# Optimization experiments

Measured on AMD Instinct MI355X. Metric: run time of the kernel, lower is better.

## Reference

```python
import jax, jax.numpy as jnp
import numpy as np

B, N, S, F = 16384, 1152, 576, 8  # batch, n_sites, n_symm, features
LOG2 = float(np.log(2.0))


def log_cosh(x):
    # numerically stable log(cosh(x)) = |x| + log1p(exp(-2|x|)) - log(2)
    a = jnp.abs(x)
    return a + jnp.log1p(jnp.exp(-2.0 * a)) - LOG2


def setup_inputs() -> dict:
    key = jax.random.key(0)
    ks = iter(jax.random.split(key, 32))
    f32 = jnp.float32
    d = {}
    d['x'] = jax.random.normal(next(ks), (B, N), dtype=f32)
    d['symmetries'] = jax.random.randint(next(ks), (S, N), 0, N, dtype=jnp.int32)
    d['corr0'] = jax.random.randint(next(ks), (576, 4), 0, N, dtype=jnp.int32)
    d['corr1'] = jax.random.randint(next(ks), (576, 4), 0, N, dtype=jnp.int32)
    d['corr2'] = jax.random.randint(next(ks), (24, 24), 0, N, dtype=jnp.int32)
    d['corr3'] = jax.random.randint(next(ks), (24, 24), 0, N, dtype=jnp.int32)
    d['corr0_symm'] = jax.random.randint(next(ks), (S, 576), 0, 576, dtype=jnp.int32)
    d['corr1_symm'] = jax.random.randint(next(ks), (S, 576), 0, 576, dtype=jnp.int32)
    d['corr2_symm'] = jax.random.randint(next(ks), (S, 24), 0, 24, dtype=jnp.int32)
    d['corr3_symm'] = jax.random.randint(next(ks), (S, 24), 0, 24, dtype=jnp.int32)
    std = 0.01
    d['hidden_bias'] = std * jax.random.normal(next(ks), (F,), dtype=f32)
    d['symm_kernel'] = std * jax.random.normal(next(ks), (F, N), dtype=f32)
    d['visible_bias'] = std * jax.random.normal(next(ks), (2,), dtype=f32)
    d['corr0_bias'] = std * jax.random.normal(next(ks), (1,), dtype=f32)
    d['corr0_kernel'] = std * jax.random.normal(next(ks), (F, 576), dtype=f32)
    d['corr1_bias'] = std * jax.random.normal(next(ks), (1,), dtype=f32)
    d['corr1_kernel'] = std * jax.random.normal(next(ks), (F, 576), dtype=f32)
    d['corr2_bias'] = std * jax.random.normal(next(ks), (1,), dtype=f32)
    d['corr2_kernel'] = std * jax.random.normal(next(ks), (F, 24), dtype=f32)
    d['corr3_bias'] = std * jax.random.normal(next(ks), (1,), dtype=f32)
    d['corr3_kernel'] = std * jax.random.normal(next(ks), (F, 24), dtype=f32)
    d['loop0_hidden_bias'] = std * jax.random.normal(next(ks), (F,), dtype=f32)
    d['loop0_kernel'] = std * jax.random.normal(next(ks), (F, 24), dtype=f32)
    d['loop1_hidden_bias'] = std * jax.random.normal(next(ks), (F,), dtype=f32)
    d['loop1_kernel'] = std * jax.random.normal(next(ks), (F, 24), dtype=f32)
    return d


def reference(x, symmetries, corr0, corr1, corr2, corr3,
              corr0_symm, corr1_symm, corr2_symm, corr3_symm,
              hidden_bias, symm_kernel, visible_bias,
              corr0_bias, corr0_kernel, corr1_bias, corr1_kernel,
              corr2_bias, corr2_kernel, corr3_bias, corr3_kernel,
              loop0_hidden_bias, loop0_kernel, loop1_hidden_bias, loop1_kernel):
    n_batch = x.shape[0]
    # symmetrized kernel: (F, S, N)
    K = jnp.take(symm_kernel, symmetries, axis=1)
    theta = jnp.einsum('bn,fsn->bfs', x, K)  # (B, F, S)
    theta = theta + hidden_bias[:, None]
    bias = jnp.sum(x.reshape(n_batch, -1, 2), axis=1) @ visible_bias  # (B,)

    correlators = [corr0, corr1, corr2, corr3]
    corr_symms = [corr0_symm, corr1_symm, corr2_symm, corr3_symm]
    corr_biases = [corr0_bias, corr1_bias, corr2_bias, corr3_bias]
    corr_kernels = [corr0_kernel, corr1_kernel, corr2_kernel, corr3_kernel]

    corr_values = []
    for corr, csym, cb, ck in zip(correlators, corr_symms, corr_biases, corr_kernels):
        ckk = jnp.take(ck, csym, axis=1)               # (F, S, C)
        cv = jnp.take(x, corr, axis=1).prod(axis=2)    # (B, C)
        corr_values.append(cv)
        theta = theta + jnp.einsum('bc,fsc->bfs', cv, ckk)
        bias = bias + cb * jnp.sum(cv, axis=1)

    out = jnp.sum(log_cosh(theta), axis=(1, 2))  # (B,)

    # last two correlators are loop correlators with dedicated hidden units
    loop_params = [(loop0_hidden_bias, loop0_kernel, corr2_symm, corr_values[2]),
                   (loop1_hidden_bias, loop1_kernel, corr3_symm, corr_values[3])]
    for lhb, lk, lsym, lv in loop_params:
        lkk = jnp.take(lk, lsym, axis=1)                      # (F, S, C)
        lt = jnp.einsum('bc,fsc->bfs', lv, lkk) + lhb[:, None]
        out = out + jnp.sum(log_cosh(lt), axis=(1, 2))

    return out + bias
```

## Files before the change

kernel.cpp:

```cpp
#include <hip/hip_runtime.h>
#include <math.h>

#define B_    16384
#define N_    1152
#define KPAD  2496
#define NKT32 78
#define KLOOP 256
#define NOUT  4608
#define NT2   18
#define LOG2F_ 0.69314718055994530942f

typedef unsigned short ushort_t;
typedef __attribute__((ext_vector_type(8))) short short8;
typedef __attribute__((ext_vector_type(4))) float floatx4;

__device__ __forceinline__ float log_cosh_f(float t) {
    float a = fabsf(t);
    return a + __logf(1.0f + __expf(-2.0f * a)) - LOG2F_;
}
__device__ __forceinline__ ushort_t bf16_rne(float f) {
    unsigned int u = __float_as_uint(f);
    return (ushort_t)((u + 0x7fffu + ((u >> 16) & 1u)) >> 16);
}
__device__ __forceinline__ float bf16_to_f(ushort_t h) {
    return __uint_as_float(((unsigned int)h) << 16);
}

typedef __attribute__((address_space(1))) const unsigned int guint;
typedef __attribute__((address_space(3))) unsigned int luint;
__device__ __forceinline__ void gload16(const ushort_t* src, ushort_t* dst) {
    __builtin_amdgcn_global_load_lds((guint*)src, (luint*)dst, 16, 0, 0);
}

__global__ __launch_bounds__(256) void build_w(
    const int* __restrict__ symm,
    const int* __restrict__ c0s, const int* __restrict__ c1s,
    const int* __restrict__ c2s, const int* __restrict__ c3s,
    const float* __restrict__ sk,
    const float* __restrict__ ck0, const float* __restrict__ ck1,
    const float* __restrict__ ck2, const float* __restrict__ ck3,
    const float* __restrict__ l0k, const float* __restrict__ l1k,
    ushort_t* __restrict__ Wb, ushort_t* __restrict__ LWb)
{
    __shared__ int idx[2352];
    const int s = blockIdx.x;
    const int tid = threadIdx.x;
    for (int i = tid; i < 1152; i += 256) idx[i] = symm[s * N_ + i];
    for (int i = tid; i < 576; i += 256) idx[1152 + i] = c0s[s * 576 + i];
    for (int i = tid; i < 576; i += 256) idx[1728 + i] = c1s[s * 576 + i];
    if (tid < 24) idx[2304 + tid] = c2s[s * 24 + tid];
    else if (tid < 48) idx[2328 + (tid - 24)] = c3s[s * 24 + (tid - 24)];
    __syncthreads();
    for (int f = 0; f < 8; ++f) {
        ushort_t* wr = Wb + (size_t)(s * 8 + f) * KPAD;
        for (int k = tid; k < KPAD; k += 256) {
            ushort_t o;
            if (k < 1152)      o = bf16_rne(sk[f * N_ + idx[k]]);
            else if (k < 1728) o = bf16_rne(ck0[f * 576 + idx[k]]);
            else if (k < 2304) o = bf16_rne(ck1[f * 576 + idx[k]]);
            else if (k < 2448) {
                int q = k - 2304, g = q / 48, c = q - g * 48;
                float w = (c < 24) ? ck2[f * 24 + idx[2304 + c]]
                                   : ck3[f * 24 + idx[2328 + (c - 24)]];
                ushort_t hi = bf16_rne(w);
                o = (g < 2) ? hi : bf16_rne(w - bf16_to_f(hi));
            } else o = 0;
            wr[k] = o;
        }
        ushort_t* lr = LWb + (size_t)(s * 8 + f) * KLOOP;
        for (int k2 = tid; k2 < KLOOP; k2 += 256) {
            int j2 = k2 >> 7, q = k2 & 127;
            ushort_t o = 0;
            if (q < 72) {
                int g = q / 24, c = q - g * 24;
                float w = j2 ? l1k[f * 24 + idx[2328 + c]]
                             : l0k[f * 24 + idx[2304 + c]];
                ushort_t hi = bf16_rne(w);
                o = (g < 2) ? hi : bf16_rne(w - bf16_to_f(hi));
            }
            lr[k2] = o;
        }
    }
}

__global__ __launch_bounds__(256) void build_cv(
    const float* __restrict__ x,
    const int* __restrict__ corr0, const int* __restrict__ corr1,
    const int* __restrict__ corr2, const int* __restrict__ corr3,
    const float* __restrict__ vb,
    const float* __restrict__ cb0, const float* __restrict__ cb1,
    const float* __restrict__ cb2, const float* __restrict__ cb3,
    ushort_t* __restrict__ XA, ushort_t* __restrict__ CVL,
    float* __restrict__ initb)
{
    __shared__ float xs[N_];
    __shared__ float red[256];
    __shared__ float cvhi[48], cvlo[48];
    const int tid = threadIdx.x;
    const int b = blockIdx.x;
    ushort_t* xr = XA + (size_t)b * KPAD;

    float bias = 0.f;
    const float vb0 = vb[0], vb1 = vb[1];
    for (int i = tid; i < N_; i += 256) {
        float v = x[(size_t)b * N_ + i];
        xs[i] = v;
        bias += v * ((i & 1) ? vb1 : vb0);
        xr[i] = bf16_rne(v);
    }
    __syncthreads();
    float s0 = 0.f, s1 = 0.f, s2 = 0.f, s3 = 0.f;
    for (int c = tid; c < 576; c += 256) {
        const int* i0 = corr0 + c * 4;
        float p = xs[i0[0]] * xs[i0[1]] * xs[i0[2]] * xs[i0[3]];
        xr[1152 + c] = bf16_rne(p); s0 += p;
        const int* i1 = corr1 + c * 4;
        float q = xs[i1[0]] * xs[i1[1]] * xs[i1[2]] * xs[i1[3]];
        xr[1728 + c] = bf16_rne(q); s1 += q;
    }
    if (tid < 48) {
        int j2 = tid / 24, c = tid - j2 * 24;
        const int* ii = (j2 ? corr3 : corr2) + c * 24;
        float p = 1.f;
        for (int j = 0; j < 24; ++j) p *= xs[ii[j]];
        float hv = bf16_to_f(bf16_rne(p));
        cvhi[tid] = hv;
        cvlo[tid] = p - hv;
        if (j2) s3 = p; else s2 = p;
    }
    __syncthreads();
    for (int i = tid; i < KPAD - 2304; i += 256) {
        ushort_t o = 0;
        if (i < 144) {
            int g = i / 48, c = i - g * 48;
            o = bf16_rne(g == 1 ? cvlo[c] : cvhi[c]);
        }
        xr[2304 + i] = o;
    }
    ushort_t* cr = CVL + (size_t)b * KLOOP;
    for (int k2 = tid; k2 < KLOOP; k2 += 256) {
        int j2 = k2 >> 7, q = k2 & 127;
        ushort_t o = 0;
        if (q < 72) {
            int g = q / 24, c = q - g * 24;
            o = bf16_rne(g == 1 ? cvlo[j2 * 24 + c] : cvhi[j2 * 24 + c]);
        }
        cr[k2] = o;
    }
    bias += cb0[0] * s0 + cb1[0] * s1 + cb2[0] * s2 + cb3[0] * s3;
    red[tid] = bias;
    __syncthreads();
    for (int off = 128; off; off >>= 1) {
        if (tid < off) red[tid] += red[tid + off];
        __syncthreads();
    }
    if (tid == 0) initb[b] = red[0];
}

__global__ __launch_bounds__(512, 4) void mfma_gemm(
    const ushort_t* __restrict__ XA, const ushort_t* __restrict__ Wb,
    const ushort_t* __restrict__ CVL, const ushort_t* __restrict__ LWb,
    const float* __restrict__ hidden_bias,
    const float* __restrict__ l0hb, const float* __restrict__ l1hb,
    float* __restrict__ partials)
{
    __shared__ __align__(16) ushort_t sh[36864];
    __shared__ float redsh[640];

    const int tid = threadIdx.x;
    const int l = tid & 63, w = tid >> 6;
    const int wm = w >> 2, wn = w & 3;
    const int lrow = l & 15, lg = l >> 4;
    const int srow = l >> 2;
    const int sgr8 = ((l & 3) ^ ((srow >> 1) & 3)) * 8;

    const int bid = blockIdx.x;
    const int swz = (bid & 7) * 288 + (bid >> 3);
    const int nt = swz >> 7, bt = swz & 127;
    const int n0 = nt * 256, b0 = bt * 128;

    const ushort_t* XAb  = XA  + (size_t)b0 * KPAD;
    const ushort_t* Wbb  = Wb  + (size_t)n0 * KPAD;
    const ushort_t* CVb  = CVL + (size_t)b0 * KLOOP;
    const ushort_t* LWbb = LWb + (size_t)n0 * KLOOP;

    floatx4 acc[4][4];

    auto STGA = [&](const ushort_t* g, int stride, int kg, int bo) {
        gload16(g + (size_t)(w * 16 + srow) * stride + kg + sgr8,
                &sh[bo + w * 16 * 32]);
    };
    auto STGB = [&](const ushort_t* g, int stride, int kg, int bo) {
#pragma unroll
        for (int i = 0; i < 2; ++i) {
            const int r0 = i * 128 + w * 16;
            gload16(g + (size_t)(r0 + srow) * stride + kg + sgr8,
                    &sh[bo + 4096 + r0 * 32]);
        }
    };

    const int ga = (lg ^ ((lrow >> 1) & 3)) * 8;
    const int abase = (wm * 64 + lrow) * 32 + ga;
    const int bbase = 4096 + (wn * 64 + lrow) * 32 + ga;

    auto TILE = [&](int bo) {
        short8 af[4], bfr[4];
#pragma unroll
        for (int mi = 0; mi < 4; ++mi)
            af[mi] = *(const short8*)&sh[bo + abase + mi * 512];
#pragma unroll
        for (int ni = 0; ni < 4; ++ni)
            bfr[ni] = *(const short8*)&sh[bo + bbase + ni * 512];
        __builtin_amdgcn_s_setprio(1);
#pragma unroll
        for (int mi = 0; mi < 4; ++mi)
#pragma unroll
            for (int ni = 0; ni < 4; ++ni)
                acc[mi][ni] = __builtin_amdgcn_mfma_f32_16x16x32_bf16(
                    af[mi], bfr[ni], acc[mi][ni], 0, 0, 0);
        __builtin_amdgcn_s_setprio(0);
    };

#pragma unroll
    for (int mi = 0; mi < 4; ++mi)
#pragma unroll
        for (int ni = 0; ni < 4; ++ni) acc[mi][ni] = (floatx4){0.f, 0.f, 0.f, 0.f};

    int c0 = 0, c1 = 12288, c2 = 24576;
    STGA(XAb, KPAD, 0, c0);  STGB(Wbb, KPAD, 0, c0);
    STGA(XAb, KPAD, 32, c1); STGB(Wbb, KPAD, 32, c1);
#pragma unroll 1
    for (int t = 0; t < NKT32 - 1; ++t) {
        asm volatile("s_waitcnt vmcnt(3)" ::: "memory");
        __builtin_amdgcn_s_barrier();
        if (t < NKT32 - 2) {
            STGA(XAb, KPAD, (t + 2) * 32, c2);
            STGB(Wbb, KPAD, (t + 2) * 32, c2);
        }
        TILE(c0);
        int tmp = c0; c0 = c1; c1 = c2; c2 = tmp;
    }
    asm volatile("s_waitcnt vmcnt(0)" ::: "memory");
    __builtin_amdgcn_s_barrier();
    TILE(c0);

    {
        const float hbv = hidden_bias[l & 7];
#pragma unroll
        for (int mi = 0; mi < 4; ++mi)
#pragma unroll
            for (int reg = 0; reg < 4; ++reg) {
                float v = 0.f;
#pragma unroll
                for (int ni = 0; ni < 4; ++ni)
                    v += log_cosh_f(acc[mi][ni][reg] + hbv);
                v += __shfl_xor(v, 1);
                v += __shfl_xor(v, 2);
                v += __shfl_xor(v, 4);
                v += __shfl_xor(v, 8);
                if (lrow == 0)
                    redsh[(wm * 64 + mi * 16 + lg * 4 + reg) * 5 + wn] = v;
            }
    }

#pragma unroll 1
    for (int j2 = 0; j2 < 2; ++j2) {
#pragma unroll
        for (int mi = 0; mi < 4; ++mi)
#pragma unroll
            for (int ni = 0; ni < 4; ++ni) acc[mi][ni] = (floatx4){0.f, 0.f, 0.f, 0.f};
        __syncthreads();
        const int kb = j2 * 128;
        STGA(CVb, KLOOP, kb, 0);          STGB(LWbb, KLOOP, kb, 0);
        STGA(CVb, KLOOP, kb + 32, 12288); STGB(LWbb, KLOOP, kb + 32, 12288);
        int m0 = 0, m1 = 12288, m2 = 24576;
#pragma unroll 1
        for (int t = 0; t < 4; ++t) {
            if (t < 3) asm volatile("s_waitcnt vmcnt(3)" ::: "memory");
            else       asm volatile("s_waitcnt vmcnt(0)" ::: "memory");
            __builtin_amdgcn_s_barrier();
            if (t < 2) {
                STGA(CVb, KLOOP, kb + (t + 2) * 32, m2);
                STGB(LWbb, KLOOP, kb + (t + 2) * 32, m2);
            }
            TILE(m0);
            int tmp = m0; m0 = m1; m1 = m2; m2 = tmp;
        }
        const float lbv = (j2 ? l1hb : l0hb)[l & 7];
#pragma unroll
        for (int mi = 0; mi < 4; ++mi)
#pragma unroll
            for (int reg = 0; reg < 4; ++reg) {
                float v = 0.f;
#pragma unroll
                for (int ni = 0; ni < 4; ++ni)
                    v += log_cosh_f(acc[mi][ni][reg] + lbv);
                v += __shfl_xor(v, 1);
                v += __shfl_xor(v, 2);
                v += __shfl_xor(v, 4);
                v += __shfl_xor(v, 8);
                if (lrow == 0)
                    redsh[(wm * 64 + mi * 16 + lg * 4 + reg) * 5 + wn] += v;
            }
    }

    __syncthreads();
    if (tid < 128) {
        float t = redsh[tid * 5 + 0] + redsh[tid * 5 + 1] +
                  redsh[tid * 5 + 2] + redsh[tid * 5 + 3];
        partials[(size_t)nt * B_ + b0 + tid] = t;
    }
}

__global__ __launch_bounds__(256) void finalize_out(
    const float* __restrict__ initb, const float* __restrict__ partials,
    float* __restrict__ out)
{
    int b = blockIdx.x * 256 + threadIdx.x;
    float s = initb[b];
#pragma unroll
    for (int t = 0; t < NT2; ++t) s += partials[(size_t)t * B_ + b];
    out[b] = s;
}

extern "C" void kernel_launch(void* const* d_in, const int* in_sizes, int n_in,
                              void* d_out, int out_size, void* d_ws, size_t ws_size,
                              hipStream_t stream) {
    const float* x    = (const float*)d_in[0];
    const int* symm   = (const int*)d_in[1];
    const int* corr0  = (const int*)d_in[2];
    const int* corr1  = (const int*)d_in[3];
    const int* corr2  = (const int*)d_in[4];
    const int* corr3  = (const int*)d_in[5];
    const int* c0s    = (const int*)d_in[6];
    const int* c1s    = (const int*)d_in[7];
    const int* c2s    = (const int*)d_in[8];
    const int* c3s    = (const int*)d_in[9];
    const float* hb   = (const float*)d_in[10];
    const float* sk   = (const float*)d_in[11];
    const float* vb   = (const float*)d_in[12];
    const float* cb0  = (const float*)d_in[13];
    const float* ck0  = (const float*)d_in[14];
    const float* cb1  = (const float*)d_in[15];
    const float* ck1  = (const float*)d_in[16];
    const float* cb2  = (const float*)d_in[17];
    const float* ck2  = (const float*)d_in[18];
    const float* cb3  = (const float*)d_in[19];
    const float* ck3  = (const float*)d_in[20];
    const float* l0hb = (const float*)d_in[21];
    const float* l0k  = (const float*)d_in[22];
    const float* l1hb = (const float*)d_in[23];
    const float* l1k  = (const float*)d_in[24];

    ushort_t* wsu = (ushort_t*)d_ws;
    ushort_t* Wb  = wsu;
    ushort_t* XA  = Wb + (size_t)NOUT * KPAD;
    ushort_t* LWb = XA + (size_t)B_ * KPAD;
    ushort_t* CVL = LWb + (size_t)NOUT * KLOOP;
    float* initb    = (float*)(CVL + (size_t)B_ * KLOOP);
    float* partials = initb + B_;

    build_w<<<576, 256, 0, stream>>>(
        symm, c0s, c1s, c2s, c3s, sk, ck0, ck1, ck2, ck3, l0k, l1k, Wb, LWb);
    build_cv<<<B_, 256, 0, stream>>>(
        x, corr0, corr1, corr2, corr3, vb, cb0, cb1, cb2, cb3, XA, CVL, initb);
    mfma_gemm<<<2304, 512, 0, stream>>>(
        XA, Wb, CVL, LWb, hb, l0hb, l1hb, partials);
    finalize_out<<<B_ / 256, 256, 0, stream>>>(initb, partials, (float*)d_out);
}
```

Baseline: 579.5 us.

## Enlarge GEMM tile to 256x256 with 32x32 MFMA and four-stage LDS pipeline

The main bf16 GEMM now computes a 256x256 output tile per block instead of 128x256, using 32x32x16 MFMA instructions with a 4x2 accumulator grid per wave. The K loop becomes a four-buffer LDS pipeline with register double-buffering of fragments, so LDS reads overlap MFMA issue. The padded K is raised to a multiple of 128 so the loop splits evenly into phases. The goal is more data reuse per loaded byte and higher MFMA throughput. In exchange it uses far more LDS, which cuts occupancy, launches half as many blocks, which may leave a tail of partly idle CUs, and adds a little padded-K work.

```diff
diff --git a/kernel.cpp b/kernel.cpp
--- a/kernel.cpp
+++ b/kernel.cpp
@@ -3,8 +3,8 @@
 
 #define B_    16384
 #define N_    1152
-#define KPAD  2496
-#define NKT32 78
+#define KPAD  2560
+#define NKT   80
 #define KLOOP 256
 #define NOUT  4608
 #define NT2   18
@@ -12,7 +12,7 @@
 
 typedef unsigned short ushort_t;
 typedef __attribute__((ext_vector_type(8))) short short8;
-typedef __attribute__((ext_vector_type(4))) float floatx4;
+typedef __attribute__((ext_vector_type(16))) float floatx16;
 
 __device__ __forceinline__ float log_cosh_f(float t) {
     float a = fabsf(t);
@@ -157,155 +157,171 @@
     if (tid == 0) initb[b] = red[0];
 }
 
-__global__ __launch_bounds__(512, 4) void mfma_gemm(
+__global__ __launch_bounds__(512, 2) void mfma_gemm(
     const ushort_t* __restrict__ XA, const ushort_t* __restrict__ Wb,
     const ushort_t* __restrict__ CVL, const ushort_t* __restrict__ LWb,
     const float* __restrict__ hidden_bias,
     const float* __restrict__ l0hb, const float* __restrict__ l1hb,
     float* __restrict__ partials)
 {
-    __shared__ __align__(16) ushort_t sh[36864];
-    __shared__ float redsh[640];
+    __shared__ __align__(16) ushort_t sh[65536];
+    __shared__ float redsh[1280];
 
     const int tid = threadIdx.x;
     const int l = tid & 63, w = tid >> 6;
     const int wm = w >> 2, wn = w & 3;
-    const int lrow = l & 15, lg = l >> 4;
+    const int l31 = l & 31, lh = l >> 5;
     const int srow = l >> 2;
     const int sgr8 = ((l & 3) ^ ((srow >> 1) & 3)) * 8;
 
     const int bid = blockIdx.x;
-    const int swz = (bid & 7) * 288 + (bid >> 3);
-    const int nt = swz >> 7, bt = swz & 127;
-    const int n0 = nt * 256, b0 = bt * 128;
+    const int swz = (bid & 7) * 144 + (bid >> 3);
+    const int nt = swz % NT2, bt = swz / NT2;
+    const int n0 = nt * 256, b0 = bt * 256;
 
     const ushort_t* XAb  = XA  + (size_t)b0 * KPAD;
     const ushort_t* Wbb  = Wb  + (size_t)n0 * KPAD;
     const ushort_t* CVb  = CVL + (size_t)b0 * KLOOP;
     const ushort_t* LWbb = LWb + (size_t)n0 * KLOOP;
 
-    floatx4 acc[4][4];
-
-    auto STGA = [&](const ushort_t* g, int stride, int kg, int bo) {
-        gload16(g + (size_t)(w * 16 + srow) * stride + kg + sgr8,
-                &sh[bo + w * 16 * 32]);
-    };
-    auto STGB = [&](const ushort_t* g, int stride, int kg, int bo) {
+    const int fsw = (l31 >> 1) & 3;
+    const int ao0 = l31 * 32 + (((0 + lh) ^ fsw) * 8);
+    const int ao1 = l31 * 32 + (((2 + lh) ^ fsw) * 8);
+    const int aBase = wm * 4096;
+    const int bBase = 8192 + wn * 2048;
+
+    floatx16 acc[4][2];
+    short8 aX[4], bX[2], aY[4], bY[2];
+
+    auto STGA = [&](const ushort_t* g, int stride, int kg, int bufbase) {
 #pragma unroll
         for (int i = 0; i < 2; ++i) {
             const int r0 = i * 128 + w * 16;
             gload16(g + (size_t)(r0 + srow) * stride + kg + sgr8,
-                    &sh[bo + 4096 + r0 * 32]);
-        }
-    };
-
-    const int ga = (lg ^ ((lrow >> 1) & 3)) * 8;
-    const int abase = (wm * 64 + lrow) * 32 + ga;
-    const int bbase = 4096 + (wn * 64 + lrow) * 32 + ga;
-
-    auto TILE = [&](int bo) {
-        short8 af[4], bfr[4];
-#pragma unroll
-        for (int mi = 0; mi < 4; ++mi)
-            af[mi] = *(const short8*)&sh[bo + abase + mi * 512];
-#pragma unroll
-        for (int ni = 0; ni < 4; ++ni)
-            bfr[ni] = *(const short8*)&sh[bo + bbase + ni * 512];
+                    &sh[bufbase + r0 * 32]);
+        }
+    };
+    auto STAGE = [&](int kg, int bufbase) {
+        STGA(XAb, KPAD, kg, bufbase);
+        STGA(Wbb, KPAD, kg, bufbase + 8192);
+    };
+    auto RD = [&](int bufbase, int ao, short8* a, short8* b) {
+#pragma unroll
+        for (int mi = 0; mi < 4; ++mi)
+            a[mi] = *(const short8*)&sh[bufbase + aBase + mi * 1024 + ao];
+#pragma unroll
+        for (int ni = 0; ni < 2; ++ni)
+            b[ni] = *(const short8*)&sh[bufbase + bBase + ni * 1024 + ao];
+    };
+    auto MM = [&](short8* a, short8* b) {
         __builtin_amdgcn_s_setprio(1);
 #pragma unroll
         for (int mi = 0; mi < 4; ++mi)
 #pragma unroll
-            for (int ni = 0; ni < 4; ++ni)
-                acc[mi][ni] = __builtin_amdgcn_mfma_f32_16x16x32_bf16(
-                    af[mi], bfr[ni], acc[mi][ni], 0, 0, 0);
+            for (int ni = 0; ni < 2; ++ni)
+                acc[mi][ni] = __builtin_amdgcn_mfma_f32_32x32x16_bf16(
+                    a[mi], b[ni], acc[mi][ni], 0, 0, 0);
         __builtin_amdgcn_s_setprio(0);
     };
-
-#pragma unroll
-    for (int mi = 0; mi < 4; ++mi)
-#pragma unroll
-        for (int ni = 0; ni < 4; ++ni) acc[mi][ni] = (floatx4){0.f, 0.f, 0.f, 0.f};
-
-    int c0 = 0, c1 = 12288, c2 = 24576;
-    STGA(XAb, KPAD, 0, c0);  STGB(Wbb, KPAD, 0, c0);
-    STGA(XAb, KPAD, 32, c1); STGB(Wbb, KPAD, 32, c1);
+    auto ZACC = [&]() {
+#pragma unroll
+        for (int mi = 0; mi < 4; ++mi)
+#pragma unroll
+            for (int ni = 0; ni < 2; ++ni)
+#pragma unroll
+                for (int r = 0; r < 16; ++r) acc[mi][ni][r] = 0.f;
+    };
+
+    ZACC();
+
+    STAGE(0, 0); STAGE(32, 16384); STAGE(64, 32768);
+    asm volatile("s_waitcnt vmcnt(8)" ::: "memory");
+    __builtin_amdgcn_sched_barrier(0);
+    __builtin_amdgcn_s_barrier();
+    RD(0, ao0, aX, bX);
+
 #pragma unroll 1
-    for (int t = 0; t < NKT32 - 1; ++t) {
-        asm volatile("s_waitcnt vmcnt(3)" ::: "memory");
-        __builtin_amdgcn_s_barrier();
-        if (t < NKT32 - 2) {
-            STGA(XAb, KPAD, (t + 2) * 32, c2);
-            STGB(Wbb, KPAD, (t + 2) * 32, c2);
-        }
-        TILE(c0);
-        int tmp = c0; c0 = c1; c1 = c2; c2 = tmp;
-    }
-    asm volatile("s_waitcnt vmcnt(0)" ::: "memory");
-    __builtin_amdgcn_s_barrier();
-    TILE(c0);
+    for (int tb = 0; tb < 19; ++tb) {
+#pragma unroll
+        for (int ph = 0; ph < 4; ++ph) {
+            const int t = tb * 4 + ph;
+            const int cb = ph * 16384;
+            const int nb = ((ph + 3) & 3) * 16384;
+            const int b1 = ((ph + 1) & 3) * 16384;
+            RD(cb, ao1, aY, bY);
+            STAGE((t + 3) * 32, nb);
+            MM(aX, bX);
+            asm volatile("s_waitcnt vmcnt(8) lgkmcnt(0)" ::: "memory");
+            __builtin_amdgcn_sched_barrier(0);
+            __builtin_amdgcn_s_barrier();
+            RD(b1, ao0, aX, bX);
+            MM(aY, bY);
+        }
+    }
+    RD(0, ao1, aY, bY); STAGE(79 * 32, 49152); MM(aX, bX);
+    asm volatile("s_waitcnt vmcnt(8) lgkmcnt(0)" ::: "memory");
+    __builtin_amdgcn_sched_barrier(0); __builtin_amdgcn_s_barrier();
+    RD(16384, ao0, aX, bX); MM(aY, bY);
+    RD(16384, ao1, aY, bY); MM(aX, bX);
+    asm volatile("s_waitcnt vmcnt(4) lgkmcnt(0)" ::: "memory");
+    __builtin_amdgcn_sched_barrier(0); __builtin_amdgcn_s_barrier();
+    RD(32768, ao0, aX, bX); MM(aY, bY);
+    RD(32768, ao1, aY, bY); MM(aX, bX);
+    asm volatile("s_waitcnt vmcnt(0) lgkmcnt(0)" ::: "memory");
+    __builtin_amdgcn_sched_barrier(0); __builtin_amdgcn_s_barrier();
+    RD(49152, ao0, aX, bX); MM(aY, bY);
+    RD(49152, ao1, aY, bY); MM(aX, bX); MM(aY, bY);
 
     {
         const float hbv = hidden_bias[l & 7];
 #pragma unroll
         for (int mi = 0; mi < 4; ++mi)
 #pragma unroll
-            for (int reg = 0; reg < 4; ++reg) {
-                float v = 0.f;
-#pragma unroll
-                for (int ni = 0; ni < 4; ++ni)
-                    v += log_cosh_f(acc[mi][ni][reg] + hbv);
-                v += __shfl_xor(v, 1);
-                v += __shfl_xor(v, 2);
-                v += __shfl_xor(v, 4);
-                v += __shfl_xor(v, 8);
-                if (lrow == 0)
-                    redsh[(wm * 64 + mi * 16 + lg * 4 + reg) * 5 + wn] = v;
+            for (int reg = 0; reg < 16; ++reg) {
+                float v = log_cosh_f(acc[mi][0][reg] + hbv)
+                        + log_cosh_f(acc[mi][1][reg] + hbv);
+                v += __shfl_xor(v, 1);  v += __shfl_xor(v, 2);
+                v += __shfl_xor(v, 4);  v += __shfl_xor(v, 8);
+                v += __shfl_xor(v, 16);
+                if (l31 == 0)
+                    redsh[(wm * 128 + mi * 32 + (reg & 3) + 8 * (reg >> 2)
+                           + 4 * lh) * 5 + wn] = v;
             }
     }
 
 #pragma unroll 1
     for (int j2 = 0; j2 < 2; ++j2) {
-#pragma unroll
-        for (int mi = 0; mi < 4; ++mi)
-#pragma unroll
-            for (int ni = 0; ni < 4; ++ni) acc[mi][ni] = (floatx4){0.f, 0.f, 0.f, 0.f};
+        ZACC();
         __syncthreads();
         const int kb = j2 * 128;
-        STGA(CVb, KLOOP, kb, 0);          STGB(LWbb, KLOOP, kb, 0);
-        STGA(CVb, KLOOP, kb + 32, 12288); STGB(LWbb, KLOOP, kb + 32, 12288);
-        int m0 = 0, m1 = 12288, m2 = 24576;
-#pragma unroll 1
-        for (int t = 0; t < 4; ++t) {
-            if (t < 3) asm volatile("s_waitcnt vmcnt(3)" ::: "memory");
-            else       asm volatile("s_waitcnt vmcnt(0)" ::: "memory");
-            __builtin_amdgcn_s_barrier();
-            if (t < 2) {
-                STGA(CVb, KLOOP, kb + (t + 2) * 32, m2);
-                STGB(LWbb, KLOOP, kb + (t + 2) * 32, m2);
+        STGA(CVb, KLOOP, kb,      0);     STGA(LWbb, KLOOP, kb,      8192);
+        STGA(CVb, KLOOP, kb + 32, 16384); STGA(LWbb, KLOOP, kb + 32, 24576);
+        STGA(CVb, KLOOP, kb + 64, 32768); STGA(LWbb, KLOOP, kb + 64, 40960);
+        STGA(CVb, KLOOP, kb + 96, 49152); STGA(LWbb, KLOOP, kb + 96, 57344);
+        __syncthreads();
+#pragma unroll
+        for (int tt = 0; tt < 4; ++tt) {
+            RD(tt * 16384, ao0, aX, bX); MM(aX, bX);
+            RD(tt * 16384, ao1, aY, bY); MM(aY, bY);
+        }
+        const float lbv = (j2 ? l1hb : l0hb)[l & 7];
+#pragma unroll
+        for (int mi = 0; mi < 4; ++mi)
+#pragma unroll
+            for (int reg = 0; reg < 16; ++reg) {
+                float v = log_cosh_f(acc[mi][0][reg] + lbv)
+                        + log_cosh_f(acc[mi][1][reg] + lbv);
+                v += __shfl_xor(v, 1);  v += __shfl_xor(v, 2);
+                v += __shfl_xor(v, 4);  v += __shfl_xor(v, 8);
+                v += __shfl_xor(v, 16);
+                if (l31 == 0)
+                    redsh[(wm * 128 + mi * 32 + (reg & 3) + 8 * (reg >> 2)
+                           + 4 * lh) * 5 + wn] += v;
             }
-            TILE(m0);
-            int tmp = m0; m0 = m1; m1 = m2; m2 = tmp;
-        }
-        const float lbv = (j2 ? l1hb : l0hb)[l & 7];
-#pragma unroll
-        for (int mi = 0; mi < 4; ++mi)
-#pragma unroll
-            for (int reg = 0; reg < 4; ++reg) {
-                float v = 0.f;
-#pragma unroll
-                for (int ni = 0; ni < 4; ++ni)
-                    v += log_cosh_f(acc[mi][ni][reg] + lbv);
-                v += __shfl_xor(v, 1);
-                v += __shfl_xor(v, 2);
-                v += __shfl_xor(v, 4);
-                v += __shfl_xor(v, 8);
-                if (lrow == 0)
-                    redsh[(wm * 64 + mi * 16 + lg * 4 + reg) * 5 + wn] += v;
-            }
-    }
-
-    __syncthreads();
-    if (tid < 128) {
+    }
+
+    __syncthreads();
+    if (tid < 256) {
         float t = redsh[tid * 5 + 0] + redsh[tid * 5 + 1] +
                   redsh[tid * 5 + 2] + redsh[tid * 5 + 3];
         partials[(size_t)nt * B_ + b0 + tid] = t;
@@ -364,7 +380,7 @@
         symm, c0s, c1s, c2s, c3s, sk, ck0, ck1, ck2, ck3, l0k, l1k, Wb, LWb);
     build_cv<<<B_, 256, 0, stream>>>(
         x, corr0, corr1, corr2, corr3, vb, cb0, cb1, cb2, cb3, XA, CVL, initb);
-    mfma_gemm<<<2304, 512, 0, stream>>>(
+    mfma_gemm<<<1152, 512, 0, stream>>>(
         XA, Wb, CVL, LWb, hb, l0hb, l1hb, partials);
     finalize_out<<<B_ / 256, 256, 0, stream>>>(initb, partials, (float*)d_out);
 }
```

New measurement: 753.0 us. 29.9% more time.

## Retile GEMM to 128x128 blocks with 4-stage LDS ring and register double-buffering

Applied to the files above, without the earlier changes.

The main GEMM kernel changes from 512-thread blocks computing 128x256 output tiles to 256-thread blocks computing 128x128 tiles, which doubles the grid and the number of N-partials. The K loop now uses a four-buffer LDS ring, loading three stages ahead, and alternates two register fragment sets so LDS reads for the next tile overlap the MFMAs of the current one. Scheduling barriers and vmcnt(4) waits pin this order. The aim is better latency hiding and occupancy, at the cost of re-reading the A operand twice as often and a longer finalize reduction.

```diff
diff --git a/kernel.cpp b/kernel.cpp
--- a/kernel.cpp
+++ b/kernel.cpp
@@ -4,10 +4,9 @@
 #define B_    16384
 #define N_    1152
 #define KPAD  2496
-#define NKT32 78
 #define KLOOP 256
 #define NOUT  4608
-#define NT2   18
+#define NT    36
 #define LOG2F_ 0.69314718055994530942f
 
 typedef unsigned short ushort_t;
@@ -157,92 +156,98 @@
     if (tid == 0) initb[b] = red[0];
 }
 
-__global__ __launch_bounds__(512, 4) void mfma_gemm(
+__global__ __launch_bounds__(256, 2) void mfma_gemm(
     const ushort_t* __restrict__ XA, const ushort_t* __restrict__ Wb,
     const ushort_t* __restrict__ CVL, const ushort_t* __restrict__ LWb,
     const float* __restrict__ hidden_bias,
     const float* __restrict__ l0hb, const float* __restrict__ l1hb,
     float* __restrict__ partials)
 {
-    __shared__ __align__(16) ushort_t sh[36864];
-    __shared__ float redsh[640];
+    __shared__ __align__(16) ushort_t sh[32768];
+    __shared__ float redsh[384];
 
     const int tid = threadIdx.x;
     const int l = tid & 63, w = tid >> 6;
-    const int wm = w >> 2, wn = w & 3;
+    const int wm = w >> 1, wn = w & 1;
     const int lrow = l & 15, lg = l >> 4;
-    const int srow = l >> 2;
-    const int sgr8 = ((l & 3) ^ ((srow >> 1) & 3)) * 8;
+    const int sgr = ((tid & 3) ^ ((tid >> 3) & 3)) * 8;
+    const int srow = tid >> 2;
+    const int wb512 = w * 512;
 
     const int bid = blockIdx.x;
-    const int swz = (bid & 7) * 288 + (bid >> 3);
+    const int swz = (bid & 7) * 576 + (bid >> 3);
     const int nt = swz >> 7, bt = swz & 127;
-    const int n0 = nt * 256, b0 = bt * 128;
-
-    const ushort_t* XAb  = XA  + (size_t)b0 * KPAD;
-    const ushort_t* Wbb  = Wb  + (size_t)n0 * KPAD;
-    const ushort_t* CVb  = CVL + (size_t)b0 * KLOOP;
-    const ushort_t* LWbb = LWb + (size_t)n0 * KLOOP;
+    const int n0 = nt * 128, b0 = bt * 128;
+
+    const ushort_t* pA0 = XA + (size_t)(b0 + srow) * KPAD + sgr;
+    const ushort_t* pA1 = pA0 + (size_t)64 * KPAD;
+    const ushort_t* pB0 = Wb + (size_t)(n0 + srow) * KPAD + sgr;
+    const ushort_t* pB1 = pB0 + (size_t)64 * KPAD;
+
+    const int oct = (lg ^ ((lrow >> 1) & 3)) * 8;
+    const int aoff = (wm * 64 + lrow) * 32 + oct;
+    const int boff = 4096 + (wn * 64 + lrow) * 32 + oct;
 
     floatx4 acc[4][4];
-
-    auto STGA = [&](const ushort_t* g, int stride, int kg, int bo) {
-        gload16(g + (size_t)(w * 16 + srow) * stride + kg + sgr8,
-                &sh[bo + w * 16 * 32]);
+    short8 RA[8], RB[8];
+
+    auto STG = [&](int bufUS, int offUS) {
+        gload16(pA0 + offUS, &sh[bufUS + 0    + wb512]);
+        gload16(pA1 + offUS, &sh[bufUS + 2048 + wb512]);
+        gload16(pB0 + offUS, &sh[bufUS + 4096 + wb512]);
+        gload16(pB1 + offUS, &sh[bufUS + 6144 + wb512]);
     };
-    auto STGB = [&](const ushort_t* g, int stride, int kg, int bo) {
-#pragma unroll
-        for (int i = 0; i < 2; ++i) {
-            const int r0 = i * 128 + w * 16;
-            gload16(g + (size_t)(r0 + srow) * stride + kg + sgr8,
-                    &sh[bo + 4096 + r0 * 32]);
-        }
+    auto RD = [&](int bufUS, short8* R) {
+#pragma unroll
+        for (int mi = 0; mi < 4; ++mi)
+            R[mi] = *(const short8*)&sh[bufUS + aoff + mi * 512];
+#pragma unroll
+        for (int ni = 0; ni < 4; ++ni)
+            R[4 + ni] = *(const short8*)&sh[bufUS + boff + ni * 512];
     };
-
-    const int ga = (lg ^ ((lrow >> 1) & 3)) * 8;
-    const int abase = (wm * 64 + lrow) * 32 + ga;
-    const int bbase = 4096 + (wn * 64 + lrow) * 32 + ga;
-
-    auto TILE = [&](int bo) {
-        short8 af[4], bfr[4];
-#pragma unroll
-        for (int mi = 0; mi < 4; ++mi)
-            af[mi] = *(const short8*)&sh[bo + abase + mi * 512];
-#pragma unroll
-        for (int ni = 0; ni < 4; ++ni)
-            bfr[ni] = *(const short8*)&sh[bo + bbase + ni * 512];
+    auto MM = [&](short8* R) {
         __builtin_amdgcn_s_setprio(1);
 #pragma unroll
         for (int mi = 0; mi < 4; ++mi)
 #pragma unroll
             for (int ni = 0; ni < 4; ++ni)
                 acc[mi][ni] = __builtin_amdgcn_mfma_f32_16x16x32_bf16(
-                    af[mi], bfr[ni], acc[mi][ni], 0, 0, 0);
+                    R[mi], R[4 + ni], acc[mi][ni], 0, 0, 0);
         __builtin_amdgcn_s_setprio(0);
     };
+#define PIPE_BAR() do { asm volatile("s_waitcnt vmcnt(4)" ::: "memory"); \
+    __builtin_amdgcn_s_barrier(); } while (0)
 
 #pragma unroll
     for (int mi = 0; mi < 4; ++mi)
 #pragma unroll
         for (int ni = 0; ni < 4; ++ni) acc[mi][ni] = (floatx4){0.f, 0.f, 0.f, 0.f};
 
-    int c0 = 0, c1 = 12288, c2 = 24576;
-    STGA(XAb, KPAD, 0, c0);  STGB(Wbb, KPAD, 0, c0);
-    STGA(XAb, KPAD, 32, c1); STGB(Wbb, KPAD, 32, c1);
+    STG(0, 0); STG(8192, 32); STG(16384, 64);
+    asm volatile("s_waitcnt vmcnt(8)" ::: "memory");
+    __builtin_amdgcn_s_barrier();
+    RD(0, RA);
+
 #pragma unroll 1
-    for (int t = 0; t < NKT32 - 1; ++t) {
-        asm volatile("s_waitcnt vmcnt(3)" ::: "memory");
-        __builtin_amdgcn_s_barrier();
-        if (t < NKT32 - 2) {
-            STGA(XAb, KPAD, (t + 2) * 32, c2);
-            STGB(Wbb, KPAD, (t + 2) * 32, c2);
-        }
-        TILE(c0);
-        int tmp = c0; c0 = c1; c1 = c2; c2 = tmp;
-    }
-    asm volatile("s_waitcnt vmcnt(0)" ::: "memory");
-    __builtin_amdgcn_s_barrier();
-    TILE(c0);
+    for (int m = 0; m < 19; ++m) {
+        RD(8192, RB);  STG(24576, 96);
+        __builtin_amdgcn_sched_barrier(0);
+        MM(RA); PIPE_BAR();
+        RD(16384, RA); STG(0, 128);
+        __builtin_amdgcn_sched_barrier(0);
+        MM(RB); PIPE_BAR();
+        RD(24576, RB); STG(8192, 160);
+        __builtin_amdgcn_sched_barrier(0);
+        MM(RA); PIPE_BAR();
+        RD(0, RA);     STG(16384, 192);
+        __builtin_amdgcn_sched_barrier(0);
+        MM(RB); PIPE_BAR();
+        pA0 += 128; pA1 += 128; pB0 += 128; pB1 += 128;
+    }
+    RD(8192, RB);
+    __builtin_amdgcn_sched_barrier(0);
+    MM(RA);
+    MM(RB);
 
     {
         const float hbv = hidden_bias[l & 7];
@@ -254,16 +259,24 @@
 #pragma unroll
                 for (int ni = 0; ni < 4; ++ni)
                     v += log_cosh_f(acc[mi][ni][reg] + hbv);
-                v += __shfl_xor(v, 1);
-                v += __shfl_xor(v, 2);
-                v += __shfl_xor(v, 4);
-                v += __shfl_xor(v, 8);
+                v += __shfl_xor(v, 1); v += __shfl_xor(v, 2);
+                v += __shfl_xor(v, 4); v += __shfl_xor(v, 8);
                 if (lrow == 0)
-                    redsh[(wm * 64 + mi * 16 + lg * 4 + reg) * 5 + wn] = v;
+                    redsh[(wm * 64 + mi * 16 + lg * 4 + reg) * 3 + wn] = v;
             }
     }
 
-#pragma unroll 1
+    const ushort_t* pC0 = CVL + (size_t)(b0 + srow) * KLOOP + sgr;
+    const ushort_t* pC1 = pC0 + (size_t)64 * KLOOP;
+    const ushort_t* pL0 = LWb + (size_t)(n0 + srow) * KLOOP + sgr;
+    const ushort_t* pL1 = pL0 + (size_t)64 * KLOOP;
+    auto STGm = [&](int bufUS, int offUS) {
+        gload16(pC0 + offUS, &sh[bufUS + 0    + wb512]);
+        gload16(pC1 + offUS, &sh[bufUS + 2048 + wb512]);
+        gload16(pL0 + offUS, &sh[bufUS + 4096 + wb512]);
+        gload16(pL1 + offUS, &sh[bufUS + 6144 + wb512]);
+    };
+#pragma unroll
     for (int j2 = 0; j2 < 2; ++j2) {
 #pragma unroll
         for (int mi = 0; mi < 4; ++mi)
@@ -271,21 +284,12 @@
             for (int ni = 0; ni < 4; ++ni) acc[mi][ni] = (floatx4){0.f, 0.f, 0.f, 0.f};
         __syncthreads();
         const int kb = j2 * 128;
-        STGA(CVb, KLOOP, kb, 0);          STGB(LWbb, KLOOP, kb, 0);
-        STGA(CVb, KLOOP, kb + 32, 12288); STGB(LWbb, KLOOP, kb + 32, 12288);
-        int m0 = 0, m1 = 12288, m2 = 24576;
-#pragma unroll 1
-        for (int t = 0; t < 4; ++t) {
-            if (t < 3) asm volatile("s_waitcnt vmcnt(3)" ::: "memory");
-            else       asm volatile("s_waitcnt vmcnt(0)" ::: "memory");
-            __builtin_amdgcn_s_barrier();
-            if (t < 2) {
-                STGA(CVb, KLOOP, kb + (t + 2) * 32, m2);
-                STGB(LWbb, KLOOP, kb + (t + 2) * 32, m2);
-            }
-            TILE(m0);
-            int tmp = m0; m0 = m1; m1 = m2; m2 = tmp;
-        }
+        STGm(0, kb); STGm(8192, kb + 32); STGm(16384, kb + 64); STGm(24576, kb + 96);
+        __syncthreads();
+        RD(0, RA);     MM(RA);
+        RD(8192, RB);  MM(RB);
+        RD(16384, RA); MM(RA);
+        RD(24576, RB); MM(RB);
         const float lbv = (j2 ? l1hb : l0hb)[l & 7];
 #pragma unroll
         for (int mi = 0; mi < 4; ++mi)
@@ -295,21 +299,19 @@
 #pragma unroll
                 for (int ni = 0; ni < 4; ++ni)
                     v += log_cosh_f(acc[mi][ni][reg] + lbv);
-                v += __shfl_xor(v, 1);
-                v += __shfl_xor(v, 2);
-                v += __shfl_xor(v, 4);
-                v += __shfl_xor(v, 8);
+                v += __shfl_xor(v, 1); v += __shfl_xor(v, 2);
+                v += __shfl_xor(v, 4); v += __shfl_xor(v, 8);
                 if (lrow == 0)
-                    redsh[(wm * 64 + mi * 16 + lg * 4 + reg) * 5 + wn] += v;
+                    redsh[(wm * 64 + mi * 16 + lg * 4 + reg) * 3 + wn] += v;
             }
     }
 
     __syncthreads();
     if (tid < 128) {
-        float t = redsh[tid * 5 + 0] + redsh[tid * 5 + 1] +
-                  redsh[tid * 5 + 2] + redsh[tid * 5 + 3];
+        float t = redsh[tid * 3 + 0] + redsh[tid * 3 + 1];
         partials[(size_t)nt * B_ + b0 + tid] = t;
     }
+#undef PIPE_BAR
 }
 
 __global__ __launch_bounds__(256) void finalize_out(
@@ -319,7 +321,7 @@
     int b = blockIdx.x * 256 + threadIdx.x;
     float s = initb[b];
 #pragma unroll
-    for (int t = 0; t < NT2; ++t) s += partials[(size_t)t * B_ + b];
+    for (int t = 0; t < NT; ++t) s += partials[(size_t)t * B_ + b];
     out[b] = s;
 }
 
@@ -364,7 +366,7 @@
         symm, c0s, c1s, c2s, c3s, sk, ck0, ck1, ck2, ck3, l0k, l1k, Wb, LWb);
     build_cv<<<B_, 256, 0, stream>>>(
         x, corr0, corr1, corr2, corr3, vb, cb0, cb1, cb2, cb3, XA, CVL, initb);
-    mfma_gemm<<<2304, 512, 0, stream>>>(
+    mfma_gemm<<<4608, 256, 0, stream>>>(
         XA, Wb, CVL, LWb, hb, l0hb, l1hb, partials);
     finalize_out<<<B_ / 256, 256, 0, stream>>>(initb, partials, (float*)d_out);
 }
```

Measured after the change: 670.2 us. +15.7%, slower.
